# Kernel tuning notes

Hardware: AMD Instinct MI355X
Metric: run time of the kernel (lower is better)

Reference implementation:

```python
import jax, jax.numpy as jnp
import numpy as np

B, T, N, D = 64, 10, 64, 4      # batch, time steps, num_vars, input_size
H = 128                          # encoder_hidden
K = 2                            # num_edge_types
EPS = 1e-5                       # BatchNorm eps
_edges = np.ones((N, N)) - np.eye(N)
SEND = jnp.asarray(np.where(_edges)[0])   # [E], E = N*(N-1)
RECV = jnp.asarray(np.where(_edges)[1])   # [E]


def _xavier(key, shape):
    std = (2.0 / (shape[0] + shape[1])) ** 0.5
    return std * jax.random.normal(key, shape, dtype=jnp.float32)


def _mlp(x, w1, b1, w2, b2, g, beta):
    # RefNRIMLP: Linear -> ELU -> (dropout p=0) -> Linear -> ELU -> BatchNorm1d
    h = jax.nn.elu(x @ w1 + b1)
    h = jax.nn.elu(h @ w2 + b2)
    flat = h.reshape(-1, h.shape[-1])  # BN over flattened (batch*objects) axis
    mu = flat.mean(0)
    var = flat.var(0)
    flat = (flat - mu) * jax.lax.rsqrt(var + EPS) * g + beta
    return flat.reshape(h.shape)


def setup_inputs() -> dict:
    key = jax.random.key(0)
    ks = jax.random.split(key, 10)
    inp = {"inputs": jax.random.normal(ks[0], (B, T, N, D), dtype=jnp.float32)}
    fan_ins = {"mlp1": T * D, "mlp2": 2 * H, "mlp3": H, "mlp4": 3 * H}
    for i, (name, nin) in enumerate(fan_ins.items()):
        k1, k2 = jax.random.split(ks[i + 1])
        inp[name + "_w1"] = _xavier(k1, (nin, H))
        inp[name + "_b1"] = jnp.full((H,), 0.1, dtype=jnp.float32)
        inp[name + "_w2"] = _xavier(k2, (H, H))
        inp[name + "_b2"] = jnp.full((H,), 0.1, dtype=jnp.float32)
        inp[name + "_g"] = jnp.ones((H,), dtype=jnp.float32)
        inp[name + "_beta"] = jnp.zeros((H,), dtype=jnp.float32)
    inp["fc_w"] = _xavier(ks[9], (H, K))
    inp["fc_b"] = jnp.full((K,), 0.1, dtype=jnp.float32)
    return inp


def reference(inputs, mlp1_w1, mlp1_b1, mlp1_w2, mlp1_b2, mlp1_g, mlp1_beta,
              mlp2_w1, mlp2_b1, mlp2_w2, mlp2_b2, mlp2_g, mlp2_beta,
              mlp3_w1, mlp3_b1, mlp3_w2, mlp3_b2, mlp3_g, mlp3_beta,
              mlp4_w1, mlp4_b1, mlp4_w2, mlp4_b2, mlp4_g, mlp4_beta,
              fc_w, fc_b):
    # [B,T,N,D] -> [B,N,T*D]
    x = jnp.transpose(inputs, (0, 2, 1, 3)).reshape(B, N, T * D)
    x = _mlp(x, mlp1_w1, mlp1_b1, mlp1_w2, mlp1_b2, mlp1_g, mlp1_beta)
    # node2edge: gather send/recv node embeddings, concat -> [B,E,2H]
    x = jnp.concatenate([x[:, SEND], x[:, RECV]], axis=-1)
    x = _mlp(x, mlp2_w1, mlp2_b1, mlp2_w2, mlp2_b2, mlp2_g, mlp2_beta)
    x_skip = x
    # edge2node: one-hot(recv).T matmul == segment_sum over recv index, then /(N-1)
    agg = jax.ops.segment_sum(jnp.swapaxes(x, 0, 1), RECV, num_segments=N)  # [N,B,H]
    x = jnp.swapaxes(agg, 0, 1) / (N - 1)  # [B,N,H]
    x = _mlp(x, mlp3_w1, mlp3_b1, mlp3_w2, mlp3_b2, mlp3_g, mlp3_beta)
    x = jnp.concatenate([x[:, SEND], x[:, RECV]], axis=-1)  # [B,E,2H]
    x = jnp.concatenate([x, x_skip], axis=-1)  # [B,E,3H]
    x = _mlp(x, mlp4_w1, mlp4_b1, mlp4_w2, mlp4_b2, mlp4_g, mlp4_beta)
    return x @ fc_w + fc_b  # logits [B, E, K]
```

## Files before the change

kernel.cpp:

```cpp
#include <hip/hip_runtime.h>

#define BN_EPS 1e-5f

using h8 = __attribute__((ext_vector_type(8))) _Float16;
using h4v = __attribute__((ext_vector_type(4))) _Float16;
using f4v = __attribute__((ext_vector_type(4))) float;

#define OFF_COEF 0
#define OFF_CVEC 1024
#define OFF_H1 4096
#define OFF_P2 528384
#define OFF_Q2 1052672
#define OFF_H3 1576960
#define OFF_P4 2101248
#define OFF_Q4 2625536
#define OFF_W2P 3149824
#define OFF_W4P 3158016
#define OFF_WCP 3166208
#define OFF_H4B 3174400
#define WS_BYTES 78757888ull

__device__ __forceinline__ float elu_f(float x) {
    return x > 0.f ? x : __expf(x) - 1.f;
}


__device__ __forceinline__ void gemm32_globalW(const float* As, int lda,
                                               const float* __restrict__ Wg, int K,
                                               float acc[2][8], int tx, int ty) {
    const float4* Wg4 = (const float4*)Wg;
#pragma unroll 4
    for (int k = 0; k < K; ++k) {
        float a0 = As[ty * lda + k];
        float a1 = As[(ty + 16) * lda + k];
        float4 wa = Wg4[k * 32 + tx];
        float4 wb = Wg4[k * 32 + 16 + tx];
        const float wv[8] = {wa.x, wa.y, wa.z, wa.w, wb.x, wb.y, wb.z, wb.w};
#pragma unroll
        for (int u = 0; u < 8; ++u) {
            acc[0][u] = fmaf(a0, wv[u], acc[0][u]);
            acc[1][u] = fmaf(a1, wv[u], acc[1][u]);
        }
    }
}

__device__ __forceinline__ void bias_elu32(const float acc[2][8],
                                           const float* __restrict__ bias,
                                           float vals[2][8], int tx) {
    int ca = 4 * tx, cb = 64 + 4 * tx;
    float bv[8] = {bias[ca], bias[ca + 1], bias[ca + 2], bias[ca + 3],
                   bias[cb], bias[cb + 1], bias[cb + 2], bias[cb + 3]};
#pragma unroll
    for (int j = 0; j < 2; ++j)
#pragma unroll
        for (int u = 0; u < 8; ++u)
            vals[j][u] = elu_f(acc[j][u] + bv[u]);
}

__device__ __forceinline__ void store_tile32(float* __restrict__ out, int row0,
                                             const float vals[2][8], int tx, int ty) {
#pragma unroll
    for (int j = 0; j < 2; ++j) {
        int r = row0 + ty + 16 * j;
        *(float4*)(out + r * 128 + 4 * tx) =
            make_float4(vals[j][0], vals[j][1], vals[j][2], vals[j][3]);
        *(float4*)(out + r * 128 + 64 + 4 * tx) =
            make_float4(vals[j][4], vals[j][5], vals[j][6], vals[j][7]);
    }
}

__device__ __forceinline__ void stats_tail32_store(const float vals[2][8], float* red,
                                                   float* __restrict__ slot, int tid,
                                                   int tx, int ty) {
    float ls[8], lq[8];
#pragma unroll
    for (int u = 0; u < 8; ++u) {
        ls[u] = vals[0][u] + vals[1][u];
        lq[u] = vals[0][u] * vals[0][u] + vals[1][u] * vals[1][u];
    }
    __syncthreads();
    int ca = 4 * tx, cb = 64 + 4 * tx;
#pragma unroll
    for (int u = 0; u < 4; ++u) {
        red[ty * 128 + ca + u] = ls[u];
        red[2048 + ty * 128 + ca + u] = lq[u];
        red[ty * 128 + cb + u] = ls[u + 4];
        red[2048 + ty * 128 + cb + u] = lq[u + 4];
    }
    __syncthreads();
    if (tid < 128) {
        float s = 0.f, q = 0.f;
#pragma unroll
        for (int t = 0; t < 16; ++t) {
            s += red[t * 128 + tid];
            q += red[2048 + t * 128 + tid];
        }
        slot[tid] = s;
        slot[128 + tid] = q;
    }
}


__device__ __forceinline__ void gemm2_gw(const _Float16* A0, const _Float16* A1,
                                         const _Float16* __restrict__ wp,
                                         f4v acc0[4][2], f4v acc1[4][2], int lane, int w) {
#pragma unroll
    for (int kc = 0; kc < 4; ++kc) {
        h8 bf0 = *(const h8*)&wp[(((w * 2 + 0) * 4 + kc) * 64 + lane) * 8];
        h8 bf1 = *(const h8*)&wp[(((w * 2 + 1) * 4 + kc) * 64 + lane) * 8];
        h8 af0[4], af1[4];
#pragma unroll
        for (int rt = 0; rt < 4; ++rt) {
            af0[rt] = *(const h8*)&A0[((rt * 4 + kc) * 64 + lane) * 8];
            af1[rt] = *(const h8*)&A1[((rt * 4 + kc) * 64 + lane) * 8];
        }
#pragma unroll
        for (int rt = 0; rt < 4; ++rt) {
            acc0[rt][0] = __builtin_amdgcn_mfma_f32_16x16x32_f16(af0[rt], bf0, acc0[rt][0], 0, 0, 0);
            acc1[rt][0] = __builtin_amdgcn_mfma_f32_16x16x32_f16(af1[rt], bf0, acc1[rt][0], 0, 0, 0);
        }
#pragma unroll
        for (int rt = 0; rt < 4; ++rt) {
            acc0[rt][1] = __builtin_amdgcn_mfma_f32_16x16x32_f16(af0[rt], bf1, acc0[rt][1], 0, 0, 0);
            acc1[rt][1] = __builtin_amdgcn_mfma_f32_16x16x32_f16(af1[rt], bf1, acc1[rt][1], 0, 0, 0);
        }
    }
}

__device__ __forceinline__ void vals_to_afrag(_Float16* Afr, const float vals[4][2][4],
                                              int lane, int w) {
    int cl = lane & 15, quad = lane >> 4;
#pragma unroll
    for (int ctl = 0; ctl < 2; ++ctl) {
        int col = (w * 2 + ctl) * 16 + cl;
        int kc = col >> 5, o = (col >> 3) & 3, j = col & 7;
#pragma unroll
        for (int rt = 0; rt < 4; ++rt)
#pragma unroll
            for (int i = 0; i < 4; ++i) {
                int m = quad * 4 + i;
                Afr[((rt * 4 + kc) * 64 + o * 16 + m) * 8 + j] = (_Float16)vals[rt][ctl][i];
            }
    }
}

__device__ __forceinline__ void stage_pair(_Float16* Afr, const float4* __restrict__ Pr,
                                           const float4* __restrict__ Qr,
                                           const float4* __restrict__ B1, int lane, int kc) {
    int rt = lane >> 4, m = lane & 15;
#pragma unroll
    for (int o = 0; o < 4; ++o) {
        int c4 = kc * 8 + o * 2;
        float4 p0 = Pr[c4], q0 = Qr[c4], bb0 = B1[c4];
        float4 p1 = Pr[c4 + 1], q1 = Qr[c4 + 1], bb1 = B1[c4 + 1];
        h8 v;
        v[0] = (_Float16)elu_f(p0.x + q0.x + bb0.x);
        v[1] = (_Float16)elu_f(p0.y + q0.y + bb0.y);
        v[2] = (_Float16)elu_f(p0.z + q0.z + bb0.z);
        v[3] = (_Float16)elu_f(p0.w + q0.w + bb0.w);
        v[4] = (_Float16)elu_f(p1.x + q1.x + bb1.x);
        v[5] = (_Float16)elu_f(p1.y + q1.y + bb1.y);
        v[6] = (_Float16)elu_f(p1.z + q1.z + bb1.z);
        v[7] = (_Float16)elu_f(p1.w + q1.w + bb1.w);
        *(h8*)&Afr[((rt * 4 + kc) * 64 + o * 16 + m) * 8] = v;
    }
}


__global__ __launch_bounds__(256) void k_mlp1p(const float* __restrict__ x,
                                               const float* __restrict__ w1,
                                               const float* __restrict__ b1,
                                               const float* __restrict__ w2,
                                               const float* __restrict__ b2,
                                               float* __restrict__ h1,
                                               float* __restrict__ slots,
                                               float* __restrict__ sums2,
                                               float* __restrict__ cvec,
                                               const float* __restrict__ w2src,
                                               _Float16* __restrict__ w2p,
                                               const float* __restrict__ w4src,
                                               _Float16* __restrict__ w4p) {
    __shared__ float Xs[32 * 44];
    __shared__ float As[32 * 132];
    int tid = threadIdx.x;
    int blk = blockIdx.x;
    if (blk >= 128) {
        if (blk < 193) {
            int i = (blk - 128) * 256 + tid;
            if (i < 16384) sums2[i] = 0.f;
            else if (i < 16512) cvec[i - 16384] = 0.f;
        } else {
            int second = blk >= 201;
            const float* src = second ? w4src : w2src;
            _Float16* wp = second ? w4p : w2p;
            int flat = (blk - (second ? 201 : 193)) * 256 + tid;
            int g = flat >> 6, L = flat & 63;
            int ct = g >> 2, kc = g & 3;
            int nn = ct * 16 + (L & 15), k0 = kc * 32 + (L >> 4) * 8;
            h8 v;
#pragma unroll
            for (int j = 0; j < 8; ++j) v[j] = (_Float16)src[(k0 + j) * 128 + nn];
            *(h8*)&wp[flat * 8] = v;
        }
        return;
    }
    int tx = tid & 15, ty = tid >> 4;
    int r0 = blk * 32;
    for (int idx = tid; idx < 32 * 40; idx += 256) {
        int r = idx / 40, k = idx - r * 40;
        int rr = r0 + r, b = rr >> 6, n = rr & 63, t = k >> 2, d = k & 3;
        Xs[r * 44 + k] = x[((b * 10 + t) * 64 + n) * 4 + d];
    }
    __syncthreads();
    float acc[2][8] = {};
    gemm32_globalW(Xs, 44, w1, 40, acc, tx, ty);
    float vals[2][8];
    bias_elu32(acc, b1, vals, tx);
    int ca = 4 * tx, cb = 64 + 4 * tx;
#pragma unroll
    for (int j = 0; j < 2; ++j) {
        int r = ty + 16 * j;
#pragma unroll
        for (int u = 0; u < 4; ++u) {
            As[r * 132 + ca + u] = vals[j][u];
            As[r * 132 + cb + u] = vals[j][u + 4];
        }
    }
    __syncthreads();
    float acc2[2][8] = {};
    gemm32_globalW(As, 132, w2, 128, acc2, tx, ty);
    float vals2[2][8];
    bias_elu32(acc2, b2, vals2, tx);
    store_tile32(h1, r0, vals2, tx, ty);
    stats_tail32_store(vals2, As, slots + blk * 256, tid, tx, ty);
}

__global__ __launch_bounds__(256) void k_pqf(const float* __restrict__ h,
                                             const float* __restrict__ slots,
                                             const float* __restrict__ g,
                                             const float* __restrict__ beta,
                                             const float* __restrict__ w,
                                             float* __restrict__ P, float* __restrict__ Q,
                                             float* __restrict__ zero4) {
    __shared__ float Cf[256];
    __shared__ float As[32 * 132];
    int tid = threadIdx.x, tx = tid & 15, ty = tid >> 4;
    int half = blockIdx.x >> 7;
    int r0 = (blockIdx.x & 127) * 32;
    if (zero4 && tid < 64) zero4[blockIdx.x * 64 + tid] = 0.f;
    if (tid < 128) {
        int c = tid;
        float s = 0.f, q = 0.f;
#pragma unroll 8
        for (int t = 0; t < 128; ++t) {
            s += slots[t * 256 + c];
            q += slots[t * 256 + 128 + c];
        }
        float mean = s * (1.f / 4096.f);
        float var = q * (1.f / 4096.f) - mean * mean;
        float a = g[c] * rsqrtf(var + BN_EPS);
        Cf[c] = a;
        Cf[128 + c] = beta[c] - mean * a;
    }
    __syncthreads();
    const float* Wg = w + half * 128 * 128;
    float* out = half ? Q : P;
    const float4* h4p = (const float4*)h;
#pragma unroll
    for (int i = 0; i < 4; ++i) {
        int f4 = tid + i * 256;
        int r = f4 >> 5, c4 = f4 & 31;
        float4 hv = h4p[(r0 + r) * 32 + c4];
        int cb = c4 * 4;
        float4 v;
        v.x = Cf[cb] * hv.x + Cf[128 + cb];
        v.y = Cf[cb + 1] * hv.y + Cf[128 + cb + 1];
        v.z = Cf[cb + 2] * hv.z + Cf[128 + cb + 2];
        v.w = Cf[cb + 3] * hv.w + Cf[128 + cb + 3];
        *(float4*)(As + r * 132 + c4 * 4) = v;
    }
    __syncthreads();
    float acc[2][8] = {};
    gemm32_globalW(As, 132, Wg, 128, acc, tx, ty);
#pragma unroll
    for (int j = 0; j < 2; ++j) {
        int r = r0 + ty + 16 * j;
        *(float4*)(out + r * 128 + 4 * tx) = make_float4(acc[j][0], acc[j][1], acc[j][2], acc[j][3]);
        *(float4*)(out + r * 128 + 64 + 4 * tx) = make_float4(acc[j][4], acc[j][5], acc[j][6], acc[j][7]);
    }
}

__global__ __launch_bounds__(256, 3) void k_mlp2agg(const float* __restrict__ P2,
                                                    const float* __restrict__ Q2,
                                                    const float* __restrict__ b1,
                                                    const _Float16* __restrict__ w2p,
                                                    const float* __restrict__ b2,
                                                    float* __restrict__ aggraw,
                                                    _Float16* __restrict__ h2,
                                                    float* __restrict__ st) {
    __shared__ _Float16 Afr0[8192];
    __shared__ _Float16 Afr1[8192];
    int tid = threadIdx.x;
    int lane = tid & 63, w = tid >> 6, cl = lane & 15, quad = lane >> 4;
    int b = blockIdx.x >> 5, j2 = blockIdx.x & 31;
    int n0 = 2 * j2, n1 = n0 + 1;
    float* stc = st + (blockIdx.x & 63) * 256;
    {
        int r = lane;
        int s0 = (r < 63) ? (r + (r >= n0 ? 1 : 0)) : n0;
        int s1i = (r < 63) ? (r + (r >= n1 ? 1 : 0)) : n1;
        const float4* B1 = (const float4*)b1;
        stage_pair(Afr0, (const float4*)(P2 + (b * 64 + s0) * 128),
                   (const float4*)(Q2 + (b * 64 + n0) * 128), B1, lane, w);
        stage_pair(Afr1, (const float4*)(P2 + (b * 64 + s1i) * 128),
                   (const float4*)(Q2 + (b * 64 + n1) * 128), B1, lane, w);
    }
    __syncthreads();
    f4v acc0[4][2], acc1[4][2];
#pragma unroll
    for (int rt = 0; rt < 4; ++rt)
#pragma unroll
        for (int c = 0; c < 2; ++c) {
            acc0[rt][c] = (f4v){0.f, 0.f, 0.f, 0.f};
            acc1[rt][c] = (f4v){0.f, 0.f, 0.f, 0.f};
        }
    gemm2_gw(Afr0, Afr1, w2p, acc0, acc1, lane, w);
    float v0[2][4][4], v1[2][4][4];
#pragma unroll
    for (int ctl = 0; ctl < 2; ++ctl) {
        int col = (w * 2 + ctl) * 16 + cl;
        float bias = b2[col];
        float a0 = 0.f, a1 = 0.f, sq = 0.f;
#pragma unroll
        for (int rt = 0; rt < 4; ++rt)
#pragma unroll
            for (int i = 0; i < 4; ++i) {
                int row = rt * 16 + quad * 4 + i;
                float va = elu_f(acc0[rt][ctl][i] + bias);
                float vb = elu_f(acc1[rt][ctl][i] + bias);
                if (row == 63) { va = 0.f; vb = 0.f; }
                v0[ctl][rt][i] = va;
                v1[ctl][rt][i] = vb;
                a0 += va;
                a1 += vb;
                sq += va * va + vb * vb;
            }
        a0 += __shfl_xor(a0, 16);
        a1 += __shfl_xor(a1, 16);
        sq += __shfl_xor(sq, 16);
        a0 += __shfl_xor(a0, 32);
        a1 += __shfl_xor(a1, 32);
        sq += __shfl_xor(sq, 32);
        if (quad == 0) {
            aggraw[(b * 64 + n0) * 128 + col] = a0;
            aggraw[(b * 64 + n1) * 128 + col] = a1;
            atomicAdd(stc + col, a0 + a1);
            atomicAdd(stc + 128 + col, sq);
        }
    }
    __syncthreads();
    unsigned short* T0 = (unsigned short*)Afr0;
    unsigned short* T1 = (unsigned short*)Afr1;
#pragma unroll
    for (int ctl = 0; ctl < 2; ++ctl) {
        int col = (w * 2 + ctl) * 16 + cl;
#pragma unroll
        for (int rt = 0; rt < 4; ++rt)
#pragma unroll
            for (int i = 0; i < 4; ++i) {
                int row = rt * 16 + quad * 4 + i;
                _Float16 ha = (_Float16)v0[ctl][rt][i];
                _Float16 hb = (_Float16)v1[ctl][rt][i];
                T0[row * 128 + col] = *(unsigned short*)&ha;
                T1[row * 128 + col] = *(unsigned short*)&hb;
            }
    }
    __syncthreads();
    {
        int rr = tid >> 2, cq = tid & 3;
        if (rr < 63) {
            int s0 = rr + (rr >= n0 ? 1 : 0);
            int e0 = s0 * 63 + (s0 > n0 ? n0 : n0 - 1);
            int s1i = rr + (rr >= n1 ? 1 : 0);
            int e1 = s1i * 63 + (s1i > n1 ? n1 : n1 - 1);
            unsigned short* d0 = (unsigned short*)h2 + ((size_t)b * 4032 + e0) * 128;
            unsigned short* d1 = (unsigned short*)h2 + ((size_t)b * 4032 + e1) * 128;
#pragma unroll
            for (int i = 0; i < 4; ++i) {
                int off = cq * 32 + i * 8;
                *(uint4*)(d0 + off) = *(uint4*)&T0[rr * 128 + off];
                *(uint4*)(d1 + off) = *(uint4*)&T1[rr * 128 + off];
            }
        }
    }
}

__global__ __launch_bounds__(128) void k_wcfin(const float* __restrict__ sums2,
                                               const float* __restrict__ g2,
                                               const float* __restrict__ be2,
                                               const float* __restrict__ w41,
                                               _Float16* __restrict__ wcp,
                                               float* __restrict__ cvec,
                                               float* __restrict__ coef2) {
    __shared__ float red[128];
    __shared__ float pr[2];
    int k = blockIdx.x, c = threadIdx.x;
    red[c] = (c < 64) ? sums2[c * 256 + k] : sums2[(c - 64) * 256 + 128 + k];
    __syncthreads();
    if (c == 0) {
        float s = 0.f, q = 0.f;
#pragma unroll 8
        for (int t = 0; t < 64; ++t) {
            s += red[t];
            q += red[64 + t];
        }
        float mean = s * (1.f / 258048.f);
        float var = q * (1.f / 258048.f) - mean * mean;
        float a = g2[k] * rsqrtf(var + BN_EPS);
        pr[0] = a;
        pr[1] = be2[k] - mean * a;
        coef2[k] = a;
        coef2[128 + k] = pr[1];
    }
    __syncthreads();
    float a2k = pr[0], sh2k = pr[1];
    float wv = w41[(256 + k) * 128 + c];
    int g = (c >> 4) * 4 + (k >> 5);
    int L = ((k >> 3) & 3) * 16 + (c & 15);
    int j = k & 7;
    wcp[(g * 64 + L) * 8 + j] = (_Float16)(a2k * wv);
    atomicAdd(&cvec[c], sh2k * wv);
}

__global__ __launch_bounds__(256) void k_mlp3(const float* __restrict__ raw,
                                              const float* __restrict__ coef2,
                                              const float* __restrict__ w1,
                                              const float* __restrict__ b1,
                                              const float* __restrict__ w2,
                                              const float* __restrict__ b2,
                                              float* __restrict__ h3,
                                              float* __restrict__ slots) {
    __shared__ float As[32 * 132];
    int tid = threadIdx.x, tx = tid & 15, ty = tid >> 4;
    int r0 = blockIdx.x * 32;
    const float4* in4 = (const float4*)raw;
    const float4* av = (const float4*)coef2;
    const float4* cv = (const float4*)(coef2 + 128);
    const float inv63 = 1.f / 63.f;
#pragma unroll
    for (int i = 0; i < 4; ++i) {
        int f4 = tid + i * 256;
        int r = f4 >> 5, c4 = f4 & 31;
        float4 hv = in4[(r0 + r) * 32 + c4];
        float4 a = av[c4], c = cv[c4];
        float4 v;
        v.x = a.x * hv.x * inv63 + c.x;
        v.y = a.y * hv.y * inv63 + c.y;
        v.z = a.z * hv.z * inv63 + c.z;
        v.w = a.w * hv.w * inv63 + c.w;
        *(float4*)(As + r * 132 + c4 * 4) = v;
    }
    __syncthreads();
    float acc[2][8] = {};
    gemm32_globalW(As, 132, w1, 128, acc, tx, ty);
    float vals[2][8];
    bias_elu32(acc, b1, vals, tx);
    __syncthreads();
    int ca = 4 * tx, cb = 64 + 4 * tx;
#pragma unroll
    for (int j = 0; j < 2; ++j) {
        int r = ty + 16 * j;
#pragma unroll
        for (int u = 0; u < 4; ++u) {
            As[r * 132 + ca + u] = vals[j][u];
            As[r * 132 + cb + u] = vals[j][u + 4];
        }
    }
    __syncthreads();
    float acc2[2][8] = {};
    gemm32_globalW(As, 132, w2, 128, acc2, tx, ty);
    float vals2[2][8];
    bias_elu32(acc2, b2, vals2, tx);
    store_tile32(h3, r0, vals2, tx, ty);
    stats_tail32_store(vals2, As, slots + blockIdx.x * 256, tid, tx, ty);
}

__global__ __launch_bounds__(256, 3) void k_mlp4r2(const _Float16* __restrict__ h2,
                                                   const float* __restrict__ P4,
                                                   const float* __restrict__ Q4,
                                                   const _Float16* __restrict__ wcp,
                                                   const float* __restrict__ cvec,
                                                   const float* __restrict__ b1,
                                                   const _Float16* __restrict__ w4p2,
                                                   const float* __restrict__ b2,
                                                   unsigned short* __restrict__ h4,
                                                   float* __restrict__ st) {
    __shared__ _Float16 Afr0[8192];
    __shared__ _Float16 Afr1[8192];
    int tid = threadIdx.x;
    int lane = tid & 63, w = tid >> 6, cl = lane & 15, quad = lane >> 4;
    unsigned t0 = 2u * blockIdx.x, t1 = t0 + 1u;
    unsigned b0 = t0 / 63, b1i = t1 / 63;
    unsigned e00 = (t0 - b0 * 63) * 64, e01 = (t1 - b1i * 63) * 64;
    int row00 = t0 * 64, row01 = t1 * 64;
    float* stc = st + (blockIdx.x & 63) * 256;
#pragma unroll
    for (int i = 0; i < 4; ++i) {
        int u = tid + i * 256;
        int r = u >> 4, cu = u & 15;
        int dst = (((r >> 4) * 4 + (cu >> 2)) * 64 + (cu & 3) * 16 + (r & 15)) * 8;
        *(h8*)&Afr0[dst] = *(const h8*)&h2[(size_t)(row00 + r) * 128 + cu * 8];
        *(h8*)&Afr1[dst] = *(const h8*)&h2[(size_t)(row01 + r) * 128 + cu * 8];
    }
    __syncthreads();
    f4v acc0[4][2], acc1[4][2];
#pragma unroll
    for (int rt = 0; rt < 4; ++rt)
#pragma unroll
        for (int c = 0; c < 2; ++c) {
            acc0[rt][c] = (f4v){0.f, 0.f, 0.f, 0.f};
            acc1[rt][c] = (f4v){0.f, 0.f, 0.f, 0.f};
        }
    gemm2_gw(Afr0, Afr1, wcp, acc0, acc1, lane, w);
    float v0[4][2][4], v1[4][2][4];
    {
        int col0 = w * 32 + cl, col1 = col0 + 16;
        float base0 = b1[col0] + cvec[col0];
        float base1 = b1[col1] + cvec[col1];
        unsigned sA0 = e00 / 63, sA1 = e01 / 63;
        unsigned baseE0 = sA0 * 63, baseE1 = sA1 * 63;
        unsigned eB0 = baseE0 + 63, eB1 = baseE1 + 63;
        unsigned sB0 = sA0 < 63u ? sA0 + 1u : sA0;
        unsigned sB1 = sA1 < 63u ? sA1 + 1u : sA1;
        const float* PA0 = P4 + (b0 * 64 + sA0) * 128;
        const float* PB0 = P4 + (b0 * 64 + sB0) * 128;
        const float* PA1 = P4 + (b1i * 64 + sA1) * 128;
        const float* PB1 = P4 + (b1i * 64 + sB1) * 128;
        float pA0c0 = PA0[col0], pA0c1 = PA0[col1];
        float pB0c0 = PB0[col0], pB0c1 = PB0[col1];
        float pA1c0 = PA1[col0], pA1c1 = PA1[col1];
        float pB1c0 = PB1[col0], pB1c1 = PB1[col1];
        const float* Qb0 = Q4 + (size_t)b0 * 8192;
        const float* Qb1 = Q4 + (size_t)b1i * 8192;
#pragma unroll
        for (int rt = 0; rt < 4; ++rt)
#pragma unroll
            for (int i = 0; i < 4; ++i) {
                int rr = rt * 16 + quad * 4 + i;
                {
                    unsigned e = e00 + rr;
                    bool hi = e >= eB0;
                    unsigned s = hi ? sB0 : sA0;
                    unsigned jj = e - (hi ? eB0 : baseE0);
                    unsigned rv = jj + (jj >= s ? 1u : 0u);
                    const float* Qr = Qb0 + rv * 128;
                    float p0 = hi ? pB0c0 : pA0c0, p1 = hi ? pB0c1 : pA0c1;
                    v0[rt][0][i] = elu_f(acc0[rt][0][i] + p0 + Qr[col0] + base0);
                    v0[rt][1][i] = elu_f(acc0[rt][1][i] + p1 + Qr[col1] + base1);
                }
                {
                    unsigned e = e01 + rr;
                    bool hi = e >= eB1;
                    unsigned s = hi ? sB1 : sA1;
                    unsigned jj = e - (hi ? eB1 : baseE1);
                    unsigned rv = jj + (jj >= s ? 1u : 0u);
                    const float* Qr = Qb1 + rv * 128;
                    float p0 = hi ? pB1c0 : pA1c0, p1 = hi ? pB1c1 : pA1c1;
                    v1[rt][0][i] = elu_f(acc1[rt][0][i] + p0 + Qr[col0] + base0);
                    v1[rt][1][i] = elu_f(acc1[rt][1][i] + p1 + Qr[col1] + base1);
                }
            }
    }
    __syncthreads();
    vals_to_afrag(Afr0, v0, lane, w);
    vals_to_afrag(Afr1, v1, lane, w);
    __syncthreads();
#pragma unroll
    for (int rt = 0; rt < 4; ++rt)
#pragma unroll
        for (int c = 0; c < 2; ++c) {
            acc0[rt][c] = (f4v){0.f, 0.f, 0.f, 0.f};
            acc1[rt][c] = (f4v){0.f, 0.f, 0.f, 0.f};
        }
    gemm2_gw(Afr0, Afr1, w4p2, acc0, acc1, lane, w);
#pragma unroll
    for (int ctl = 0; ctl < 2; ++ctl) {
        int col = (w * 2 + ctl) * 16 + cl;
        float bias = b2[col];
        float s1 = 0.f, s2 = 0.f;
#pragma unroll
        for (int rt = 0; rt < 4; ++rt)
#pragma unroll
            for (int i = 0; i < 4; ++i) {
                float va = elu_f(acc0[rt][ctl][i] + bias);
                float vb = elu_f(acc1[rt][ctl][i] + bias);
                v0[rt][ctl][i] = va;
                v1[rt][ctl][i] = vb;
                s1 += va + vb;
                s2 += va * va + vb * vb;
            }
        s1 += __shfl_xor(s1, 16);
        s2 += __shfl_xor(s2, 16);
        s1 += __shfl_xor(s1, 32);
        s2 += __shfl_xor(s2, 32);
        if (quad == 0) {
            atomicAdd(stc + col, s1);
            atomicAdd(stc + 128 + col, s2);
        }
    }
    __syncthreads();
    unsigned short* T0 = (unsigned short*)Afr0;
    unsigned short* T1 = (unsigned short*)Afr1;
#pragma unroll
    for (int ctl = 0; ctl < 2; ++ctl) {
        int col = (w * 2 + ctl) * 16 + cl;
#pragma unroll
        for (int rt = 0; rt < 4; ++rt)
#pragma unroll
            for (int i = 0; i < 4; ++i) {
                int rr = rt * 16 + quad * 4 + i;
                _Float16 ha = (_Float16)v0[rt][ctl][i];
                _Float16 hb = (_Float16)v1[rt][ctl][i];
                T0[rr * 128 + col] = *(unsigned short*)&ha;
                T1[rr * 128 + col] = *(unsigned short*)&hb;
            }
    }
    __syncthreads();
    {
        int rr = tid >> 2, cq = tid & 3;
#pragma unroll
        for (int i = 0; i < 4; ++i) {
            int off = rr * 128 + cq * 32 + i * 8;
            *(uint4*)(h4 + (size_t)row00 * 128 + off) = *(uint4*)&T0[off];
            *(uint4*)(h4 + (size_t)row01 * 128 + off) = *(uint4*)&T1[off];
        }
    }
}

__global__ __launch_bounds__(256) void k_outf(const unsigned short* __restrict__ h4,
                                              const float* __restrict__ sums4,
                                              const float* __restrict__ g4,
                                              const float* __restrict__ be4,
                                              const float* __restrict__ fcw,
                                              const float* __restrict__ fcb,
                                              float* __restrict__ out) {
    __shared__ float Cf[256];
    int tid = threadIdx.x;
    if (tid < 128) {
        int c = tid;
        float s = 0.f, q = 0.f;
#pragma unroll 8
        for (int t = 0; t < 64; ++t) {
            s += sums4[t * 256 + c];
            q += sums4[t * 256 + 128 + c];
        }
        float mean = s * (1.f / 258048.f);
        float var = q * (1.f / 258048.f) - mean * mean;
        float a = g4[c] * rsqrtf(var + BN_EPS);
        Cf[c] = a;
        Cf[128 + c] = be4[c] - mean * a;
    }
    __syncthreads();
    int lane = tid & 31, rsub = tid >> 5;
    const float4* Wp = (const float4*)(fcw + lane * 8);
    float4 w01 = Wp[0], w23 = Wp[1];
    float fb0 = fcb[0], fb1 = fcb[1];
    float a0 = Cf[lane * 4], a1 = Cf[lane * 4 + 1], a2 = Cf[lane * 4 + 2], a3 = Cf[lane * 4 + 3];
    float c0 = Cf[128 + lane * 4], c1 = Cf[128 + lane * 4 + 1];
    float c2 = Cf[128 + lane * 4 + 2], c3 = Cf[128 + lane * 4 + 3];
    size_t base = (size_t)blockIdx.x * 256;
#pragma unroll 4
    for (int it = 0; it < 32; ++it) {
        size_t row = base + it * 8 + rsub;
        h4v hv = ((const h4v*)(h4 + row * 128))[lane];
        float x0 = a0 * (float)hv[0] + c0;
        float x1 = a1 * (float)hv[1] + c1;
        float x2 = a2 * (float)hv[2] + c2;
        float x3 = a3 * (float)hv[3] + c3;
        float s0 = x0 * w01.x + x1 * w01.z + x2 * w23.x + x3 * w23.z;
        float s1 = x0 * w01.y + x1 * w01.w + x2 * w23.y + x3 * w23.w;
#pragma unroll
        for (int off = 16; off > 0; off >>= 1) {
            s0 += __shfl_down(s0, off, 32);
            s1 += __shfl_down(s1, off, 32);
        }
        if (lane == 0) {
            out[row * 2] = s0 + fb0;
            out[row * 2 + 1] = s1 + fb1;
        }
    }
}


extern "C" void kernel_launch(void* const* d_in, const int* in_sizes, int n_in,
                              void* d_out, int out_size, void* d_ws, size_t ws_size,
                              hipStream_t stream) {
    const float* x = (const float*)d_in[0];
    const float* m1_w1 = (const float*)d_in[1];
    const float* m1_b1 = (const float*)d_in[2];
    const float* m1_w2 = (const float*)d_in[3];
    const float* m1_b2 = (const float*)d_in[4];
    const float* m1_g = (const float*)d_in[5];
    const float* m1_be = (const float*)d_in[6];
    const float* m2_w1 = (const float*)d_in[7];
    const float* m2_b1 = (const float*)d_in[8];
    const float* m2_w2 = (const float*)d_in[9];
    const float* m2_b2 = (const float*)d_in[10];
    const float* m2_g = (const float*)d_in[11];
    const float* m2_be = (const float*)d_in[12];
    const float* m3_w1 = (const float*)d_in[13];
    const float* m3_b1 = (const float*)d_in[14];
    const float* m3_w2 = (const float*)d_in[15];
    const float* m3_b2 = (const float*)d_in[16];
    const float* m3_g = (const float*)d_in[17];
    const float* m3_be = (const float*)d_in[18];
    const float* m4_w1 = (const float*)d_in[19];
    const float* m4_b1 = (const float*)d_in[20];
    const float* m4_w2 = (const float*)d_in[21];
    const float* m4_b2 = (const float*)d_in[22];
    const float* m4_g = (const float*)d_in[23];
    const float* m4_be = (const float*)d_in[24];
    const float* fc_w = (const float*)d_in[25];
    const float* fc_b = (const float*)d_in[26];
    float* out = (float*)d_out;

    float* W = (float*)d_ws;
    float* coef2 = W + OFF_COEF;
    float* cvec = W + OFF_CVEC;
    float* h1 = W + OFF_H1;
    float* aggraw = h1;
    float* sums4 = h1;
    float* P2 = W + OFF_P2;
    float* sums3 = P2;
    float* Q2 = W + OFF_Q2;
    float* h3 = W + OFF_H3;
    float* sums1 = h3;
    float* P4 = W + OFF_P4;
    float* sums2 = P4;
    float* Q4 = W + OFF_Q4;
    _Float16* w2p2 = (_Float16*)(W + OFF_W2P);
    _Float16* w4p2 = (_Float16*)(W + OFF_W4P);
    _Float16* wcp = (_Float16*)(W + OFF_WCP);
    _Float16* h2f = (_Float16*)(W + OFF_H4B);
    unsigned short* h4b = (unsigned short*)(W + OFF_H4B);

    if (ws_size < WS_BYTES) return;

    k_mlp1p<<<209, 256, 0, stream>>>(x, m1_w1, m1_b1, m1_w2, m1_b2, h1, sums1,
                                     sums2, cvec, m2_w2, w2p2, m4_w2, w4p2);
    k_pqf<<<256, 256, 0, stream>>>(h1, sums1, m1_g, m1_be, m2_w1, P2, Q2, nullptr);
    k_mlp2agg<<<2048, 256, 0, stream>>>(P2, Q2, m2_b1, w2p2, m2_b2, aggraw, h2f, sums2);
    k_wcfin<<<128, 128, 0, stream>>>(sums2, m2_g, m2_be, m4_w1, wcp, cvec, coef2);
    k_mlp3<<<128, 256, 0, stream>>>(aggraw, coef2, m3_w1, m3_b1, m3_w2, m3_b2, h3, sums3);
    k_pqf<<<256, 256, 0, stream>>>(h3, sums3, m3_g, m3_be, m4_w1, P4, Q4, sums4);
    k_mlp4r2<<<2016, 256, 0, stream>>>(h2f, P4, Q4, wcp, cvec, m4_b1, w4p2, m4_b2,
                                       h4b, sums4);
    k_outf<<<1008, 256, 0, stream>>>(h4b, sums4, m4_g, m4_be, fc_w, fc_b, out);
}
```

Baseline: 337.4 us.

## Store h4 in MFMA fragment layout, use LDS direct loads, fold BN into fc

k_mlp4r2 now fills its LDS A-fragments with global_load_lds DMA straight from h2. It writes h4 directly in the MFMA accumulator fragment order, so the LDS transpose pass and two barriers go away. k_outf is rewritten to read that fragment layout and folds the BatchNorm scale and shift into the fc weights and a constant. k_mlp2agg pads its LDS transpose stride to 144 to avoid bank conflicts. The risk is a tighter coupling between the kernels' layouts and the correctness of the direct-to-LDS load addressing.

After: 335.8 us. About the same (-0.5%).

```diff
diff --git a/kernel.cpp b/kernel.cpp
--- a/kernel.cpp
+++ b/kernel.cpp
@@ -298,8 +298,8 @@
                                                     float* __restrict__ aggraw,
                                                     _Float16* __restrict__ h2,
                                                     float* __restrict__ st) {
-    __shared__ _Float16 Afr0[8192];
-    __shared__ _Float16 Afr1[8192];
+    __shared__ __align__(16) _Float16 Afr0[9216];
+    __shared__ __align__(16) _Float16 Afr1[9216];
     int tid = threadIdx.x;
     int lane = tid & 63, w = tid >> 6, cl = lane & 15, quad = lane >> 4;
     int b = blockIdx.x >> 5, j2 = blockIdx.x & 31;
@@ -371,8 +371,8 @@
                 int row = rt * 16 + quad * 4 + i;
                 _Float16 ha = (_Float16)v0[ctl][rt][i];
                 _Float16 hb = (_Float16)v1[ctl][rt][i];
-                T0[row * 128 + col] = *(unsigned short*)&ha;
-                T1[row * 128 + col] = *(unsigned short*)&hb;
+                T0[row * 144 + col] = *(unsigned short*)&ha;
+                T1[row * 144 + col] = *(unsigned short*)&hb;
             }
     }
     __syncthreads();
@@ -388,8 +388,8 @@
 #pragma unroll
             for (int i = 0; i < 4; ++i) {
                 int off = cq * 32 + i * 8;
-                *(uint4*)(d0 + off) = *(uint4*)&T0[rr * 128 + off];
-                *(uint4*)(d1 + off) = *(uint4*)&T1[rr * 128 + off];
+                *(uint4*)(d0 + off) = *(uint4*)&T0[rr * 144 + off];
+                *(uint4*)(d1 + off) = *(uint4*)&T1[rr * 144 + off];
             }
         }
     }
@@ -495,22 +495,27 @@
                                                    const float* __restrict__ b2,
                                                    unsigned short* __restrict__ h4,
                                                    float* __restrict__ st) {
-    __shared__ _Float16 Afr0[8192];
-    __shared__ _Float16 Afr1[8192];
+    __shared__ __align__(16) _Float16 Afr0[8192];
+    __shared__ __align__(16) _Float16 Afr1[8192];
     int tid = threadIdx.x;
     int lane = tid & 63, w = tid >> 6, cl = lane & 15, quad = lane >> 4;
     unsigned t0 = 2u * blockIdx.x, t1 = t0 + 1u;
     unsigned b0 = t0 / 63, b1i = t1 / 63;
     unsigned e00 = (t0 - b0 * 63) * 64, e01 = (t1 - b1i * 63) * 64;
-    int row00 = t0 * 64, row01 = t1 * 64;
     float* stc = st + (blockIdx.x & 63) * 256;
-#pragma unroll
-    for (int i = 0; i < 4; ++i) {
-        int u = tid + i * 256;
-        int r = u >> 4, cu = u & 15;
-        int dst = (((r >> 4) * 4 + (cu >> 2)) * 64 + (cu & 3) * 16 + (r & 15)) * 8;
-        *(h8*)&Afr0[dst] = *(const h8*)&h2[(size_t)(row00 + r) * 128 + cu * 8];
-        *(h8*)&Afr1[dst] = *(const h8*)&h2[(size_t)(row01 + r) * 128 + cu * 8];
+    {
+        const _Float16* hb = h2 + (size_t)t0 * 8192;
+#pragma unroll
+        for (int j = 0; j < 8; ++j) {
+            int win = w * 8 + j;
+            int rk = win & 15;
+            const _Float16* src = hb + (size_t)((win >> 4) * 64 + (rk >> 2) * 16 + cl) * 128
+                                     + (rk & 3) * 32 + quad * 8;
+            _Float16* dst = ((win & 16) ? Afr1 : Afr0) + rk * 512;
+            __builtin_amdgcn_global_load_lds((const __attribute__((address_space(1))) void*)src,
+                                             (__attribute__((address_space(3))) void*)dst,
+                                             16, 0, 0);
+        }
     }
     __syncthreads();
     f4v acc0[4][2], acc1[4][2];
@@ -608,31 +613,24 @@
             atomicAdd(stc + 128 + col, s2);
         }
     }
-    __syncthreads();
-    unsigned short* T0 = (unsigned short*)Afr0;
-    unsigned short* T1 = (unsigned short*)Afr1;
-#pragma unroll
-    for (int ctl = 0; ctl < 2; ++ctl) {
-        int col = (w * 2 + ctl) * 16 + cl;
-#pragma unroll
-        for (int rt = 0; rt < 4; ++rt)
-#pragma unroll
-            for (int i = 0; i < 4; ++i) {
-                int rr = rt * 16 + quad * 4 + i;
-                _Float16 ha = (_Float16)v0[rt][ctl][i];
-                _Float16 hb = (_Float16)v1[rt][ctl][i];
-                T0[rr * 128 + col] = *(unsigned short*)&ha;
-                T1[rr * 128 + col] = *(unsigned short*)&hb;
+    {
+        unsigned short* o0 = h4 + (size_t)t0 * 8192;
+        unsigned short* o1 = h4 + (size_t)t1 * 8192;
+#pragma unroll
+        for (int ctl = 0; ctl < 2; ++ctl) {
+            int cg = w * 2 + ctl;
+#pragma unroll
+            for (int rt = 0; rt < 4; ++rt) {
+                int idx = ((cg * 4 + rt) * 4 + quad) * 64 + cl * 4;
+                h4v a, bvv;
+#pragma unroll
+                for (int i = 0; i < 4; ++i) {
+                    a[i] = (_Float16)v0[rt][ctl][i];
+                    bvv[i] = (_Float16)v1[rt][ctl][i];
+                }
+                *(h4v*)(o0 + idx) = a;
+                *(h4v*)(o1 + idx) = bvv;
             }
-    }
-    __syncthreads();
-    {
-        int rr = tid >> 2, cq = tid & 3;
-#pragma unroll
-        for (int i = 0; i < 4; ++i) {
-            int off = rr * 128 + cq * 32 + i * 8;
-            *(uint4*)(h4 + (size_t)row00 * 128 + off) = *(uint4*)&T0[off];
-            *(uint4*)(h4 + (size_t)row01 * 128 + off) = *(uint4*)&T1[off];
         }
     }
 }
@@ -644,7 +642,9 @@
                                               const float* __restrict__ fcw,
                                               const float* __restrict__ fcb,
                                               float* __restrict__ out) {
-    __shared__ float Cf[256];
+    __shared__ float U0[128];
+    __shared__ float U1[128];
+    __shared__ float Cp[4];
     int tid = threadIdx.x;
     if (tid < 128) {
         int c = tid;
@@ -657,36 +657,62 @@
         float mean = s * (1.f / 258048.f);
         float var = q * (1.f / 258048.f) - mean * mean;
         float a = g4[c] * rsqrtf(var + BN_EPS);
-        Cf[c] = a;
-        Cf[128 + c] = be4[c] - mean * a;
-    }
-    __syncthreads();
-    int lane = tid & 31, rsub = tid >> 5;
-    const float4* Wp = (const float4*)(fcw + lane * 8);
-    float4 w01 = Wp[0], w23 = Wp[1];
-    float fb0 = fcb[0], fb1 = fcb[1];
-    float a0 = Cf[lane * 4], a1 = Cf[lane * 4 + 1], a2 = Cf[lane * 4 + 2], a3 = Cf[lane * 4 + 3];
-    float c0 = Cf[128 + lane * 4], c1 = Cf[128 + lane * 4 + 1];
-    float c2 = Cf[128 + lane * 4 + 2], c3 = Cf[128 + lane * 4 + 3];
-    size_t base = (size_t)blockIdx.x * 256;
-#pragma unroll 4
-    for (int it = 0; it < 32; ++it) {
-        size_t row = base + it * 8 + rsub;
-        h4v hv = ((const h4v*)(h4 + row * 128))[lane];
-        float x0 = a0 * (float)hv[0] + c0;
-        float x1 = a1 * (float)hv[1] + c1;
-        float x2 = a2 * (float)hv[2] + c2;
-        float x3 = a3 * (float)hv[3] + c3;
-        float s0 = x0 * w01.x + x1 * w01.z + x2 * w23.x + x3 * w23.z;
-        float s1 = x0 * w01.y + x1 * w01.w + x2 * w23.y + x3 * w23.w;
-#pragma unroll
-        for (int off = 16; off > 0; off >>= 1) {
-            s0 += __shfl_down(s0, off, 32);
-            s1 += __shfl_down(s1, off, 32);
-        }
-        if (lane == 0) {
-            out[row * 2] = s0 + fb0;
-            out[row * 2 + 1] = s1 + fb1;
+        float sh = be4[c] - mean * a;
+        float w0 = fcw[2 * c], w1 = fcw[2 * c + 1];
+        U0[c] = a * w0;
+        U1[c] = a * w1;
+        float p0 = sh * w0, p1 = sh * w1;
+#pragma unroll
+        for (int off = 1; off < 64; off <<= 1) {
+            p0 += __shfl_xor(p0, off);
+            p1 += __shfl_xor(p1, off);
+        }
+        if ((tid & 63) == 0) {
+            Cp[(tid >> 6) * 2] = p0;
+            Cp[(tid >> 6) * 2 + 1] = p1;
+        }
+    }
+    __syncthreads();
+    float C0 = Cp[0] + Cp[2] + fcb[0];
+    float C1 = Cp[1] + Cp[3] + fcb[1];
+    int lane = tid & 63, w = tid >> 6;
+    int quad = lane >> 4, cl = lane & 15;
+    float u0r[8], u1r[8];
+#pragma unroll
+    for (int cg = 0; cg < 8; ++cg) {
+        u0r[cg] = U0[cg * 16 + cl];
+        u1r[cg] = U1[cg * 16 + cl];
+    }
+    size_t tile = (size_t)blockIdx.x * 4 + w;
+    const unsigned short* hb = h4 + tile * 8192;
+#pragma unroll
+    for (int rt = 0; rt < 4; ++rt) {
+        float s00 = 0.f, s01 = 0.f, s02 = 0.f, s03 = 0.f;
+        float s10 = 0.f, s11 = 0.f, s12 = 0.f, s13 = 0.f;
+#pragma unroll
+        for (int cg = 0; cg < 8; ++cg) {
+            h4v hv = *(const h4v*)(hb + ((cg * 4 + rt) * 4 + quad) * 64 + cl * 4);
+            float u0 = u0r[cg], u1 = u1r[cg];
+            float x0 = (float)hv[0], x1 = (float)hv[1];
+            float x2 = (float)hv[2], x3 = (float)hv[3];
+            s00 = fmaf(x0, u0, s00); s01 = fmaf(x1, u0, s01);
+            s02 = fmaf(x2, u0, s02); s03 = fmaf(x3, u0, s03);
+            s10 = fmaf(x0, u1, s10); s11 = fmaf(x1, u1, s11);
+            s12 = fmaf(x2, u1, s12); s13 = fmaf(x3, u1, s13);
+        }
+#pragma unroll
+        for (int off = 1; off < 16; off <<= 1) {
+            s00 += __shfl_xor(s00, off); s01 += __shfl_xor(s01, off);
+            s02 += __shfl_xor(s02, off); s03 += __shfl_xor(s03, off);
+            s10 += __shfl_xor(s10, off); s11 += __shfl_xor(s11, off);
+            s12 += __shfl_xor(s12, off); s13 += __shfl_xor(s13, off);
+        }
+        if (cl == 0) {
+            size_t R = tile * 64 + rt * 16 + quad * 4;
+            *(float4*)(out + R * 2) =
+                make_float4(s00 + C0, s10 + C1, s01 + C0, s11 + C1);
+            *(float4*)(out + R * 2 + 4) =
+                make_float4(s02 + C0, s12 + C1, s03 + C0, s13 + C1);
         }
     }
 }
```
